# Optimization experiments

Measured on AMD Instinct MI355X. Metric: run time of the kernel, lower is better.

## Reference

```python
import jax, jax.numpy as jnp
import numpy as np

R, B, HQ, HK, D, DV = 4, 4, 32, 8, 128, 128   # ranks, batch, q heads, kv heads, head dims
N = 4096                                       # max kv tokens per rank (page_size=1)
PAGES = B * N                                  # pages per rank's cache
SCALE = 1.0 / float(np.sqrt(D))


def setup_inputs() -> dict:
    key = jax.random.key(0)
    k0, k1, k2, k3 = jax.random.split(key, 4)
    q = jax.random.normal(k0, (B, HQ, D), dtype=jnp.float32)
    k_cache = jax.random.normal(k1, (R, PAGES, HK, D), dtype=jnp.float32)
    v_cache = jax.random.normal(k2, (R, PAGES, HK, DV), dtype=jnp.float32)
    # each rank's shard length per batch row, in [N//2, N]
    global_kv_lens = jax.random.randint(k3, (R, B), N // 2, N + 1).astype(jnp.int32)
    # page_size=1: block_table[r, b, t] = page index of token t of row b on rank r
    block_table = jnp.broadcast_to(
        jnp.arange(PAGES, dtype=jnp.int32).reshape(B, N), (R, B, N)
    )
    return dict(q=q, k_cache=k_cache, v_cache=v_cache,
                global_kv_lens=global_kv_lens, block_table=block_table)


def _rank_partial(q, k_cache, v_cache, lens, bt):
    """Intra-rank paged GQA flash-decode: returns normalized partial output and LSE.
    q: [B,HQ,D]  k_cache/v_cache: [PAGES,HK,D]  lens: [B]  bt: [B,N]
    """
    k = k_cache[bt]                      # [B,N,HK,D] paged gather
    v = v_cache[bt]                      # [B,N,HK,DV]
    G = HQ // HK
    qg = q.reshape(B, HK, G, D)
    s = jnp.einsum('bkgd,bnkd->bkgn', qg, k) * SCALE   # [B,HK,G,N]
    valid = jnp.arange(N) < lens[:, None]              # [B,N]
    s = jnp.where(valid[:, None, None, :], s, -jnp.inf)
    m = jnp.max(s, axis=-1, keepdims=True)             # online-softmax max
    p = jnp.exp(s - m)
    l = jnp.sum(p, axis=-1)                            # [B,HK,G]
    out = jnp.einsum('bkgn,bnkd->bkgd', p, v) / l[..., None]
    lse = m[..., 0] + jnp.log(l)                       # the '+1' slot of output_combine
    return out.reshape(B, HQ, DV), lse.reshape(B, HQ)


def reference(q, k_cache, v_cache, global_kv_lens, block_table):
    # per-rank partial states (simulates intra-rank kernel on every rank)
    out_r, lse_r = jax.vmap(_rank_partial, in_axes=(None, 0, 0, 0, 0))(
        q, k_cache, v_cache, global_kv_lens, block_table)   # [R,B,HQ,DV], [R,B,HQ]
    # inter-rank combine (simulates allgather + rescale kernel)
    has_kv = (global_kv_lens > 0)[:, :, None]                # [R,B,1]
    lse_r = jnp.where(has_kv, lse_r, -jnp.inf)
    M = jnp.max(lse_r, axis=0)                               # [B,HQ]
    w = jnp.where(has_kv, jnp.exp(lse_r - M[None]), 0.0)     # [R,B,HQ]
    final = jnp.einsum('rbh,rbhd->bhd', w, out_r) / jnp.sum(w, axis=0)[..., None]
    return final
```

## Files before the change

### kernel.cpp

```cpp
#include <hip/hip_runtime.h>

namespace {

constexpr int R = 4, B = 4, HQ = 32, HK = 8, G = 4, D = 128, DV = 128;
constexpr int N = 4096, PAGES = 16384;
constexpr int NSPLIT = 32;
constexpr float SCALE = 0.08838834764831845f;

__device__ __forceinline__ float xsh(float v, int m) { return __shfl_xor(v, m, 64); }

__device__ __forceinline__ void phase(const float (&q0)[G][4],
                                      const float4 k, const float4 v, bool valid,
                                      float (&l)[G], float (&acc)[G][4]) {
  float s[G];
#pragma unroll
  for (int g = 0; g < G; ++g)
    s[g] = q0[g][0]*k.x + q0[g][1]*k.y + q0[g][2]*k.z + q0[g][3]*k.w;
#pragma unroll
  for (int mk = 1; mk <= 16; mk <<= 1) {
#pragma unroll
    for (int g = 0; g < G; ++g) s[g] += xsh(s[g], mk);
  }
#pragma unroll
  for (int g = 0; g < G; ++g) {
    float p = __expf(valid ? s[g] : -INFINITY);
    l[g] += p;
    acc[g][0] += p * v.x; acc[g][1] += p * v.y;
    acc[g][2] += p * v.z; acc[g][3] += p * v.w;
  }
}

__global__ __launch_bounds__(256, 4)
void gqa_partial_kernel(const float* __restrict__ q,
                        const float* __restrict__ kc,
                        const float* __restrict__ vc,
                        const int*   __restrict__ lens,
                        const int*   __restrict__ bt,
                        float* __restrict__ pout,
                        float* __restrict__ plse)
{
  const int lane = threadIdx.x & 63;
  const int w    = threadIdx.x >> 6;
  const int jsl  = w & 1;
  const int half = w >> 1;
  const int j32  = lane & 31;
  const int tt   = lane >> 5;

  const int bx    = blockIdx.x;
  const int rb    = ((bx >> 8) << 1) | jsl;
  const int h     = bx & 7;
  const int split = (bx >> 3) & 31;
  const int b = rb & 3, r = rb >> 2;

  const int len = lens[rb];
  const int s0  = (len * split) >> 5;
  const int e0  = (len * (split + 1)) >> 5;
  const int mid = (s0 + e0) >> 1;
  const int a   = half ? mid : s0;
  const int e   = half ? e0  : mid;
  const int sz  = e - a, szm1 = sz - 1;
  const int nt  = (sz + 1) >> 1;

  const int* btp = bt + rb * N + a;
  const float* kbase = kc + (size_t)r * PAGES * HK * D  + h * D  + j32 * 4;
  const float* vbase = vc + (size_t)r * PAGES * HK * DV + h * DV + j32 * 4;

  auto TOK = [&](int x) { return min(2 * x + tt, szm1); };
  auto KVLD = [&](float4& kk, float4& vv, int pg) {
    kk = *reinterpret_cast<const float4*>(kbase + (size_t)pg * (HK * D));
    vv = *reinterpret_cast<const float4*>(vbase + (size_t)pg * (HK * DV));
  };

  const float* qb = q + ((b * HQ + h * G) * D) + j32 * 4;
  float q0[G][4];
#pragma unroll
  for (int g = 0; g < G; ++g) {
    float4 qv = *reinterpret_cast<const float4*>(qb + g * D);
    q0[g][0] = qv.x * SCALE; q0[g][1] = qv.y * SCALE;
    q0[g][2] = qv.z * SCALE; q0[g][3] = qv.w * SCALE;
  }

  float l[G], acc[G][4];
#pragma unroll
  for (int g = 0; g < G; ++g) {
    l[g] = 0.f;
    acc[g][0] = acc[g][1] = acc[g][2] = acc[g][3] = 0.f;
  }

  float4 k0, v0, k1, v1, k2, v2;
  KVLD(k0, v0, btp[TOK(0)]);
  KVLD(k1, v1, btp[TOK(1)]);
  int p2 = btp[TOK(2)];
  int p0 = btp[TOK(3)];
  int p1 = 0;

  int j = 0;
  while (j + 2 < nt) {
    p1 = btp[TOK(j + 4)];  KVLD(k2, v2, p2);
    phase(q0, k0, v0, (2*j + tt) < sz, l, acc);

    p2 = btp[TOK(j + 5)];  KVLD(k0, v0, p0);
    phase(q0, k1, v1, (2*(j+1) + tt) < sz, l, acc);

    p0 = btp[TOK(j + 6)];  KVLD(k1, v1, p1);
    phase(q0, k2, v2, (2*(j+2) + tt) < sz, l, acc);

    j += 3;
  }
  if (j     < nt) phase(q0, k0, v0, (2*j     + tt) < sz, l, acc);
  if (j + 1 < nt) phase(q0, k1, v1, (2*(j+1) + tt) < sz, l, acc);

#pragma unroll
  for (int g = 0; g < G; ++g) {
    l[g] += xsh(l[g], 32);
#pragma unroll
    for (int k4 = 0; k4 < 4; ++k4) acc[g][k4] += xsh(acc[g][k4], 32);
  }

  __shared__ __align__(16) float lacc[2][G][DV];
  __shared__ float ll[2][G];
  if (half == 1) {
    if (tt == 0) {
#pragma unroll
      for (int g = 0; g < G; ++g) {
        float4 o; o.x = acc[g][0]; o.y = acc[g][1]; o.z = acc[g][2]; o.w = acc[g][3];
        *reinterpret_cast<float4*>(&lacc[jsl][g][j32 * 4]) = o;
      }
    }
    if (lane < G) ll[jsl][lane] = l[lane == 1 ? 1 : (lane == 2 ? 2 : (lane == 3 ? 3 : 0))];
  }
  __syncthreads();
  if (half == 1) return;

#pragma unroll
  for (int g = 0; g < G; ++g) {
    float4 o = *reinterpret_cast<const float4*>(&lacc[jsl][g][j32 * 4]);
    acc[g][0] += o.x; acc[g][1] += o.y; acc[g][2] += o.z; acc[g][3] += o.w;
    l[g] += ll[jsl][g];
  }

  size_t pbase = (((size_t)(rb * HK + h) * G) * NSPLIT + split) * (size_t)DV;
  if (tt == 0) {
#pragma unroll
    for (int g = 0; g < G; ++g) {
      float inv = 1.0f / l[g];
      float4 o;
      o.x = acc[g][0] * inv; o.y = acc[g][1] * inv;
      o.z = acc[g][2] * inv; o.w = acc[g][3] * inv;
      *reinterpret_cast<float4*>(pout + pbase + (size_t)g * NSPLIT * DV + j32 * 4) = o;
    }
  }
  if (lane < G) {
    float lv =            __logf(l[0]);
    lv = (lane == 1) ? __logf(l[1]) : lv;
    lv = (lane == 2) ? __logf(l[2]) : lv;
    lv = (lane == 3) ? __logf(l[3]) : lv;
    plse[((size_t)(rb * HK + h) * G + lane) * NSPLIT + split] = lv;
  }
}

__global__ __launch_bounds__(128)
void gqa_combine_kernel(const float* __restrict__ pout,
                        const float* __restrict__ plse,
                        float* __restrict__ out)
{
  int bx = blockIdx.x;
  int g  = bx % G;
  int h  = (bx / G) % HK;
  int b  = bx / (G * HK);

  int tid  = threadIdx.x;
  int lane = tid & 63;
  int wv   = tid >> 6;

  __shared__ float ws[R * NSPLIT];
  __shared__ float red[4];

  int rr = tid >> 5, cc = tid & 31;
  float lse = plse[((size_t)((rr * B + b) * HK + h) * G + g) * NSPLIT + cc];

  float v = lse;
#pragma unroll
  for (int mk = 32; mk >= 1; mk >>= 1) v = fmaxf(v, __shfl_xor(v, mk, 64));
  if (lane == 0) red[wv] = v;
  __syncthreads();
  float M = fmaxf(red[0], red[1]);

  float w = __expf(lse - M);
  ws[tid] = w;
  float sv = w;
#pragma unroll
  for (int mk = 32; mk >= 1; mk >>= 1) sv += __shfl_xor(sv, mk, 64);
  if (lane == 0) red[2 + wv] = sv;
  __syncthreads();
  float W = red[2] + red[3];

  float acc = 0.f;
  const float* pp = pout + (((size_t)(b * HK + h) * G + g) * NSPLIT) * (size_t)DV + tid;
#pragma unroll 4
  for (int i = 0; i < R * NSPLIT; ++i) {
    int r2 = i >> 5, c2 = i & 31;
    size_t off = ((size_t)r2 * B * HK * G * NSPLIT + (size_t)c2) * (size_t)DV;
    acc += ws[i] * pp[off];
  }
  out[((size_t)b * HQ + h * G + g) * DV + tid] = acc / W;
}

}

extern "C" void kernel_launch(void* const* d_in, const int* in_sizes, int n_in,
                              void* d_out, int out_size, void* d_ws, size_t ws_size,
                              hipStream_t stream)
{
  const float* q    = (const float*)d_in[0];
  const float* kc   = (const float*)d_in[1];
  const float* vc   = (const float*)d_in[2];
  const int*   lens = (const int*)d_in[3];
  const int*   bt   = (const int*)d_in[4];
  float* out = (float*)d_out;

  float* pout = (float*)d_ws;
  float* plse = pout + (size_t)R * B * HK * G * NSPLIT * DV;

  hipLaunchKernelGGL(gqa_partial_kernel, dim3(2048), dim3(256), 0, stream,
                     q, kc, vc, lens, bt, pout, plse);

  hipLaunchKernelGGL(gqa_combine_kernel, dim3(B * HK * G), dim3(128), 0, stream,
                     pout, plse, out);
}
```

Measured before the change: 91.66 us.

## Add length-proportional token-chunk kernel covering all KV heads per block

Adds a new partial kernel in which each block processes a contiguous token chunk for all 8 KV heads. A full page row of 4 KB is read per token, which should coalesce better than per-head 512-byte reads. Blocks are assigned to (rank, batch) rows in proportion to their sequence lengths, so load is balanced across variable lengths and the validity masking is no longer needed. A new combine kernel merges the variable number of chunks per row. The new path runs only when the workspace is large enough and falls back to the old kernels otherwise. Each chunk spans fewer tokens, so each one pays its own setup and writes more partial output.

```diff
diff --git a/kernel.cpp b/kernel.cpp
--- a/kernel.cpp
+++ b/kernel.cpp
@@ -3,11 +3,192 @@
 namespace {
 
 constexpr int R = 4, B = 4, HQ = 32, HK = 8, G = 4, D = 128, DV = 128;
-constexpr int N = 4096, PAGES = 16384;
+constexpr int N = 4096, PAGES = 16384, RBN = 16;
+constexpr int NBLK = 2048;
+constexpr int MAXG = NBLK + RBN;
 constexpr int NSPLIT = 32;
 constexpr float SCALE = 0.08838834764831845f;
 
 __device__ __forceinline__ float xsh(float v, int m) { return __shfl_xor(v, m, 64); }
+
+__device__ __forceinline__ void fp_phase(const float (&q0)[G][4],
+                                         const float4 k, const float4 v,
+                                         float (&l)[G], float (&acc)[G][4]) {
+  float s[G];
+#pragma unroll
+  for (int g = 0; g < G; ++g)
+    s[g] = q0[g][0]*k.x + q0[g][1]*k.y + q0[g][2]*k.z + q0[g][3]*k.w;
+#pragma unroll
+  for (int mk = 1; mk <= 16; mk <<= 1) {
+#pragma unroll
+    for (int g = 0; g < G; ++g) s[g] += xsh(s[g], mk);
+  }
+#pragma unroll
+  for (int g = 0; g < G; ++g) {
+    float p = __expf(s[g]);
+    l[g] += p;
+    acc[g][0] += p*v.x; acc[g][1] += p*v.y;
+    acc[g][2] += p*v.z; acc[g][3] += p*v.w;
+  }
+}
+
+__global__ __launch_bounds__(256, 4)
+void gqa_fullpage_kernel(const float* __restrict__ q,
+                         const float* __restrict__ kc,
+                         const float* __restrict__ vc,
+                         const int*   __restrict__ lens,
+                         const int*   __restrict__ bt,
+                         float* __restrict__ pout,
+                         float* __restrict__ plse)
+{
+  const int gblk = blockIdx.x;
+
+  int T = 0;
+#pragma unroll
+  for (int i = 0; i < RBN; ++i) T += lens[i];
+  int rb = -1, cidx = 0, len = 0, ncl = 0, run = 0;
+#pragma unroll
+  for (int i = 0; i < RBN; ++i) {
+    int li  = lens[i];
+    int nci = (NBLK * li + T - 1) / T;
+    if (rb < 0 && gblk < run + nci) { rb = i; cidx = gblk - run; len = li; ncl = nci; }
+    run += nci;
+  }
+  if (rb < 0) return;
+
+  const int t0 = (len * cidx) / ncl;
+  const int t1 = (len * (cidx + 1)) / ncl;
+  const int sz = t1 - t0, szm1 = sz - 1;
+
+  const int b = rb & 3, r = rb >> 2;
+  const int tid  = threadIdx.x;
+  const int head = tid >> 5;
+  const int j    = tid & 31;
+
+  const int* btp = bt + rb * N + t0;
+  const float* kb = kc + (size_t)r * PAGES * (HK * D)  + tid * 4;
+  const float* vb = vc + (size_t)r * PAGES * (HK * DV) + tid * 4;
+
+  auto BTL = [&](int x) { return btp[min(x, szm1)]; };
+  auto KVLD = [&](float4& kk, float4& vv, int pg) {
+    kk = *reinterpret_cast<const float4*>(kb + (size_t)pg * (HK * D));
+    vv = *reinterpret_cast<const float4*>(vb + (size_t)pg * (HK * DV));
+  };
+
+  const float* qb = q + ((b * HQ + head * G) * D) + j * 4;
+  float q0[G][4];
+#pragma unroll
+  for (int g = 0; g < G; ++g) {
+    float4 qv = *reinterpret_cast<const float4*>(qb + g * D);
+    q0[g][0] = qv.x * SCALE; q0[g][1] = qv.y * SCALE;
+    q0[g][2] = qv.z * SCALE; q0[g][3] = qv.w * SCALE;
+  }
+
+  float l[G], acc[G][4];
+#pragma unroll
+  for (int g = 0; g < G; ++g) {
+    l[g] = 0.f;
+    acc[g][0] = acc[g][1] = acc[g][2] = acc[g][3] = 0.f;
+  }
+
+  float4 k0, v0, k1, v1, k2, v2;
+  KVLD(k0, v0, BTL(0));
+  KVLD(k1, v1, BTL(1));
+  int p2 = BTL(2), p0 = BTL(3), p1 = 0;
+
+  int t = 0;
+  while (t + 2 < sz) {
+    p1 = BTL(t + 4);  KVLD(k2, v2, p2);  fp_phase(q0, k0, v0, l, acc);
+    p2 = BTL(t + 5);  KVLD(k0, v0, p0);  fp_phase(q0, k1, v1, l, acc);
+    p0 = BTL(t + 6);  KVLD(k1, v1, p1);  fp_phase(q0, k2, v2, l, acc);
+    t += 3;
+  }
+  if (t     < sz) fp_phase(q0, k0, v0, l, acc);
+  if (t + 1 < sz) fp_phase(q0, k1, v1, l, acc);
+
+  size_t base = ((size_t)gblk * HQ + head * G) * DV;
+#pragma unroll
+  for (int g = 0; g < G; ++g) {
+    float inv = 1.0f / l[g];
+    float4 o;
+    o.x = acc[g][0]*inv; o.y = acc[g][1]*inv;
+    o.z = acc[g][2]*inv; o.w = acc[g][3]*inv;
+    *reinterpret_cast<float4*>(pout + base + (size_t)g * DV + j * 4) = o;
+  }
+  if (j == 0) {
+#pragma unroll
+    for (int g = 0; g < G; ++g)
+      plse[(size_t)gblk * HQ + head * G + g] = __logf(l[g]);
+  }
+}
+
+__global__ __launch_bounds__(128)
+void gqa_fp_combine(const float* __restrict__ pout,
+                    const float* __restrict__ plse,
+                    const int*   __restrict__ lens,
+                    float* __restrict__ out)
+{
+  const int bx  = blockIdx.x;
+  const int b   = bx >> 5;
+  const int hq  = bx & 31;
+  const int tid = threadIdx.x;
+  const int lane = tid & 63, wv = tid >> 6;
+
+  int T = 0;
+#pragma unroll
+  for (int i = 0; i < RBN; ++i) T += lens[i];
+  int preA[4], ncA[4]; int run = 0;
+#pragma unroll
+  for (int i = 0; i < RBN; ++i) {
+    int nci = (NBLK * lens[i] + T - 1) / T;
+    if ((i & 3) == b) { preA[i >> 2] = run; ncA[i >> 2] = nci; }
+    run += nci;
+  }
+  int ofs[4];
+  ofs[0] = 0; ofs[1] = ncA[0]; ofs[2] = ofs[1] + ncA[1]; ofs[3] = ofs[2] + ncA[2];
+
+  __shared__ float w[1024];
+  __shared__ float red[4];
+
+  float m = -INFINITY;
+#pragma unroll
+  for (int r2 = 0; r2 < 4; ++r2)
+    for (int i = tid; i < ncA[r2]; i += 128)
+      m = fmaxf(m, plse[(size_t)(preA[r2] + i) * HQ + hq]);
+#pragma unroll
+  for (int mk = 32; mk >= 1; mk >>= 1) m = fmaxf(m, __shfl_xor(m, mk, 64));
+  if (lane == 0) red[wv] = m;
+  __syncthreads();
+  const float M = fmaxf(red[0], red[1]);
+
+  float s = 0.f;
+#pragma unroll
+  for (int r2 = 0; r2 < 4; ++r2)
+    for (int i = tid; i < ncA[r2]; i += 128) {
+      float ww = __expf(plse[(size_t)(preA[r2] + i) * HQ + hq] - M);
+      w[ofs[r2] + i] = ww; s += ww;
+    }
+#pragma unroll
+  for (int mk = 32; mk >= 1; mk >>= 1) s += __shfl_xor(s, mk, 64);
+  if (lane == 0) red[2 + wv] = s;
+  __syncthreads();
+  const float W = red[2] + red[3];
+
+  float a = 0.f;
+#pragma unroll
+  for (int r2 = 0; r2 < 4; ++r2) {
+    const float* pp = pout + ((size_t)preA[r2] * HQ + hq) * DV + tid;
+    const int n = ncA[r2], o = ofs[r2];
+    int i = 0;
+    for (; i + 4 <= n; i += 4) {
+      float x0 = pp[(size_t)(i+0) * HQ * DV], x1 = pp[(size_t)(i+1) * HQ * DV];
+      float x2 = pp[(size_t)(i+2) * HQ * DV], x3 = pp[(size_t)(i+3) * HQ * DV];
+      a += w[o+i]*x0 + w[o+i+1]*x1 + w[o+i+2]*x2 + w[o+i+3]*x3;
+    }
+    for (; i < n; ++i) a += w[o+i] * pp[(size_t)i * HQ * DV];
+  }
+  out[((size_t)b * HQ + hq) * DV + tid] = a / W;
+}
 
 __device__ __forceinline__ void phase(const float (&q0)[G][4],
                                       const float4 k, const float4 v, bool valid,
@@ -98,13 +279,10 @@
   while (j + 2 < nt) {
     p1 = btp[TOK(j + 4)];  KVLD(k2, v2, p2);
     phase(q0, k0, v0, (2*j + tt) < sz, l, acc);
-
     p2 = btp[TOK(j + 5)];  KVLD(k0, v0, p0);
     phase(q0, k1, v1, (2*(j+1) + tt) < sz, l, acc);
-
     p0 = btp[TOK(j + 6)];  KVLD(k1, v1, p1);
     phase(q0, k2, v2, (2*(j+2) + tt) < sz, l, acc);
-
     j += 3;
   }
   if (j     < nt) phase(q0, k0, v0, (2*j     + tt) < sz, l, acc);
@@ -219,12 +397,21 @@
   const int*   bt   = (const int*)d_in[4];
   float* out = (float*)d_out;
 
-  float* pout = (float*)d_ws;
-  float* plse = pout + (size_t)R * B * HK * G * NSPLIT * DV;
-
-  hipLaunchKernelGGL(gqa_partial_kernel, dim3(2048), dim3(256), 0, stream,
-                     q, kc, vc, lens, bt, pout, plse);
-
-  hipLaunchKernelGGL(gqa_combine_kernel, dim3(B * HK * G), dim3(128), 0, stream,
-                     pout, plse, out);
-}
+  const size_t need = (size_t)MAXG * HQ * DV * 4 + (size_t)MAXG * HQ * 4;
+
+  if (ws_size >= need) {
+    float* pout = (float*)d_ws;
+    float* plse = pout + (size_t)MAXG * HQ * DV;
+    hipLaunchKernelGGL(gqa_fullpage_kernel, dim3(MAXG), dim3(256), 0, stream,
+                       q, kc, vc, lens, bt, pout, plse);
+    hipLaunchKernelGGL(gqa_fp_combine, dim3(B * HQ), dim3(128), 0, stream,
+                       pout, plse, lens, out);
+  } else {
+    float* pout = (float*)d_ws;
+    float* plse = pout + (size_t)R * B * HK * G * NSPLIT * DV;
+    hipLaunchKernelGGL(gqa_partial_kernel, dim3(2048), dim3(256), 0, stream,
+                       q, kc, vc, lens, bt, pout, plse);
+    hipLaunchKernelGGL(gqa_combine_kernel, dim3(B * HK * G), dim3(128), 0, stream,
+                       pout, plse, out);
+  }
+}
```

New measurement: 114.3 us. 24.7% more time.
